# Optimization experiments

Measured on AMD Instinct MI355X. Metric: run time of the kernel, lower is better.

The kernel has to match this reference:

```python
import jax, jax.numpy as jnp
import numpy as np

DIL = 2  # dilation_rate from init_kwargs

def _conv_same(x, w, b, dil=DIL):
    # x: [B,H,W,C], w: [kh,kw,Cin,Cout] (HWIO), 'same' padding with dilation, stride 1
    y = jax.lax.conv_general_dilated(
        x, w, window_strides=(1, 1), padding='SAME',
        rhs_dilation=(dil, dil),
        dimension_numbers=('NHWC', 'HWIO', 'NHWC'))
    return y + b


def setup_inputs() -> dict:
    key = jax.random.key(0)
    ks = jax.random.split(key, 4)
    B, H, W, C = 8, 128, 256, 64
    F, VF, K = 64, 64, 3
    X = jax.random.normal(ks[0], (B, H, W, C), dtype=jnp.float32)
    Wq = jax.random.normal(ks[1], (K, K, C, F), dtype=jnp.float32) * 0.05
    Wk = jax.random.normal(ks[2], (K, K, C, F), dtype=jnp.float32) * 0.05
    Wv = jax.random.normal(ks[3], (K, K, C, VF), dtype=jnp.float32) * 0.05
    bq = jnp.zeros((F,), jnp.float32)
    bk = jnp.zeros((F,), jnp.float32)
    bv = jnp.zeros((VF,), jnp.float32)
    return {"X": X, "Wq": Wq, "bq": bq, "Wk": Wk, "bk": bk, "Wv": Wv, "bv": bv}


def reference(X, Wq, bq, Wk, bk, Wv, bv):
    q = _conv_same(X, Wq, bq)   # [B,H,W,F]
    k = _conv_same(X, Wk, bk)   # [B,H,W,F]
    v = _conv_same(X, Wv, bv)   # [B,H,W,VF]
    # tf.matmul(q, k, transpose_b=True): batch dims [B,H], attend along W. No scaling.
    scores = jnp.einsum('bhqf,bhkf->bhqk', q, k)          # [B,H,W,W]
    attn = jax.nn.softmax(scores, axis=-1)
    return jnp.einsum('bhqk,bhkf->bhqf', attn, v)         # [B,H,W,VF]
```

## Files before the change

### kernel.cpp

```cpp
#include <hip/hip_runtime.h>

#define B_ 8
#define H_ 128
#define W_ 256
#define C_ 64
#define F_ 64

typedef __attribute__((ext_vector_type(8))) short short8;
typedef __attribute__((ext_vector_type(8))) _Float16 half8;
typedef __attribute__((ext_vector_type(4))) float f32x4;

__device__ __forceinline__ unsigned short f2h(float x) {
    _Float16 h = (_Float16)x;
    return __builtin_bit_cast(unsigned short, h);
}

__device__ __forceinline__ f32x4 mfma16(short8 a, short8 b, f32x4 c) {
    return __builtin_amdgcn_mfma_f32_16x16x32_f16(
        __builtin_bit_cast(half8, a), __builtin_bit_cast(half8, b), c, 0, 0, 0);
}

__global__ void wprep_kernel(const float* __restrict__ Wq,
                             const float* __restrict__ Wk,
                             const float* __restrict__ Wv,
                             unsigned short* __restrict__ Wt)
{
    int e = blockIdx.x * 256 + threadIdx.x;
    int c   = e & 63;
    int f   = (e >> 6) % 192;
    int tap = e / 12288;
    const float* src = (f < 64) ? Wq : (f < 128) ? Wk : Wv;
    int ff = f & 63;
    float v = src[(long)tap * 4096 + c * 64 + ff];
    Wt[e] = f2h(v);
}

#define XST 36
#define WST 36

__global__ __launch_bounds__(256, 3) void conv_mfma(
    const float* __restrict__ X, const unsigned short* __restrict__ Wt,
    const float* __restrict__ bq, const float* __restrict__ bk,
    const float* __restrict__ bv,
    unsigned short* __restrict__ Qg, unsigned short* __restrict__ Kg,
    unsigned short* __restrict__ Vtg)
{
    __shared__ __align__(16) unsigned short Xs[260 * XST];
    __shared__ __align__(16) unsigned short Wls[288 * WST];

    const int tid  = threadIdx.x;
    const int wv   = tid >> 6;
    const int lane = tid & 63;
    const int l15  = lane & 15;
    const int g    = lane >> 4;
    const int bx   = blockIdx.x;
    const int bh   = bx >> 1;
    const int half = bx & 1;
    const int b    = bh >> 7;
    const int h    = bh & 127;

    f32x4 acc[4][6];
    #pragma unroll
    for (int mt = 0; mt < 4; ++mt)
        #pragma unroll
        for (int nt = 0; nt < 6; ++nt)
            acc[mt][nt] = (f32x4){0.f, 0.f, 0.f, 0.f};

    for (int kh = 0; kh < 3; ++kh) {
        const int ih = h + 2 * (kh - 1);
        if ((unsigned)ih >= (unsigned)H_) continue;
        const float* Xr = X + ((long)(b * H_ + ih) * W_) * C_;

        for (int cc = 0; cc < 2; ++cc) {
            const int c0 = cc * 32;
            __syncthreads();

            for (int e = tid; e < 260 * 8; e += 256) {
                const int row = e >> 3, c4 = e & 7;
                const int w_in = row - 2;
                float4 val = make_float4(0.f, 0.f, 0.f, 0.f);
                if ((unsigned)w_in < (unsigned)W_)
                    val = *(const float4*)(Xr + (long)w_in * 64 + c0 + c4 * 4);
                uint2 p;
                p.x = (unsigned)f2h(val.x) | ((unsigned)f2h(val.y) << 16);
                p.y = (unsigned)f2h(val.z) | ((unsigned)f2h(val.w) << 16);
                *(uint2*)(Xs + row * XST + c4 * 4) = p;
            }
            for (int e = tid; e < 1152; e += 256) {
                const int c8 = e & 3, f = (e >> 2) % 96, kw = e / 384;
                uint4 d = *(const uint4*)(Wt +
                    (((long)(kh * 3 + kw) * 192 + half * 96 + f) * 64 + c0 + c8 * 8));
                *(uint4*)(Wls + (kw * 96 + f) * WST + c8 * 8) = d;
            }
            __syncthreads();

            #pragma unroll
            for (int kw = 0; kw < 3; ++kw) {
                short8 bfrag[6];
                #pragma unroll
                for (int nt = 0; nt < 6; ++nt)
                    bfrag[nt] = *(const short8*)(Wls +
                        (kw * 96 + nt * 16 + l15) * WST + g * 8);
                #pragma unroll
                for (int mt = 0; mt < 4; ++mt) {
                    const int row = wv * 64 + mt * 16 + l15 + 2 * kw;
                    short8 a = *(const short8*)(Xs + row * XST + g * 8);
                    #pragma unroll
                    for (int nt = 0; nt < 6; ++nt)
                        acc[mt][nt] = mfma16(a, bfrag[nt], acc[mt][nt]);
                }
            }
        }
    }

    float bias[6];
    #pragma unroll
    for (int nt = 0; nt < 6; ++nt) {
        const int fp = half * 96 + nt * 16 + l15;
        bias[nt] = (fp < 64) ? bq[fp] : (fp < 128) ? bk[fp - 64] : bv[fp - 128];
    }
    #pragma unroll
    for (int mt = 0; mt < 4; ++mt) {
        const int wrow = wv * 64 + mt * 16 + 4 * g;
        #pragma unroll
        for (int nt = 0; nt < 6; ++nt) {
            const int fp = half * 96 + nt * 16 + l15;
            if (fp < 128) {
                unsigned short* dst = (fp < 64) ? Qg : Kg;
                const int f = fp & 63;
                #pragma unroll
                for (int r = 0; r < 4; ++r)
                    dst[((long)bh * 256 + wrow + r) * 64 + f] =
                        f2h(acc[mt][nt][r] + bias[nt]);
            } else {
                const int f = fp - 128;
                uint2 p;
                p.x = (unsigned)f2h(acc[mt][nt][0] + bias[nt]) |
                      ((unsigned)f2h(acc[mt][nt][1] + bias[nt]) << 16);
                p.y = (unsigned)f2h(acc[mt][nt][2] + bias[nt]) |
                      ((unsigned)f2h(acc[mt][nt][3] + bias[nt]) << 16);
                *(uint2*)(Vtg + ((long)bh * 64 + f) * 256 + wrow) = p;
            }
        }
    }
}

#define KST 72
#define PST 72

__global__ __launch_bounds__(256, 2) void attn_mfma(
    const unsigned short* __restrict__ Qg, const unsigned short* __restrict__ Kg,
    const unsigned short* __restrict__ Vtg, float* __restrict__ Out)
{
    __shared__ __align__(16) unsigned short Ks[2][64 * KST];
    __shared__ __align__(16) unsigned short Vts[2][64 * KST];
    __shared__ __align__(16) unsigned short Ps[4][64 * PST];

    const int tid  = threadIdx.x;
    const int wv   = tid >> 6;
    const int lane = tid & 63;
    const int l15  = lane & 15;
    const int g    = lane >> 4;
    const long bh  = blockIdx.x;

    short8 qf[4][2];
    #pragma unroll
    for (int mt = 0; mt < 4; ++mt)
        #pragma unroll
        for (int kt = 0; kt < 2; ++kt)
            qf[mt][kt] = *(const short8*)(Qg +
                (bh * 256 + wv * 64 + mt * 16 + l15) * 64 + (kt * 4 + g) * 8);

    const int srow = tid >> 2, sch = (tid & 3) * 16;

    {
        const unsigned short* kp = Kg + (bh * 256 + srow) * 64 + sch;
        const unsigned short* vp = Vtg + (bh * 64 + srow) * 256 + sch;
        *(uint4*)(Ks[0] + srow * KST + sch)     = *(const uint4*)(kp);
        *(uint4*)(Ks[0] + srow * KST + sch + 8) = *(const uint4*)(kp + 8);
        *(uint4*)(Vts[0] + srow * KST + sch)     = *(const uint4*)(vp);
        *(uint4*)(Vts[0] + srow * KST + sch + 8) = *(const uint4*)(vp + 8);
    }

    f32x4 po[4][4], lacc[4];
    float mrun[4][4];
    #pragma unroll
    for (int mt = 0; mt < 4; ++mt) {
        #pragma unroll
        for (int nt = 0; nt < 4; ++nt) po[mt][nt] = (f32x4){0.f,0.f,0.f,0.f};
        lacc[mt] = (f32x4){0.f,0.f,0.f,0.f};
        #pragma unroll
        for (int r = 0; r < 4; ++r) mrun[mt][r] = -3.0e38f;
    }

    short8 ones;
    #pragma unroll
    for (int i = 0; i < 8; ++i) ones[i] = (short)0x3C00;

    unsigned short* Pw = &Ps[wv][0];

    for (int t = 0; t < 4; ++t) {
        __syncthreads();
        const int cur = t & 1;
        if (t < 3) {
            const int nx = cur ^ 1, t0 = (t + 1) * 64;
            const unsigned short* kp = Kg + (bh * 256 + t0 + srow) * 64 + sch;
            const unsigned short* vp = Vtg + (bh * 64 + srow) * 256 + t0 + sch;
            *(uint4*)(Ks[nx] + srow * KST + sch)     = *(const uint4*)(kp);
            *(uint4*)(Ks[nx] + srow * KST + sch + 8) = *(const uint4*)(kp + 8);
            *(uint4*)(Vts[nx] + srow * KST + sch)     = *(const uint4*)(vp);
            *(uint4*)(Vts[nx] + srow * KST + sch + 8) = *(const uint4*)(vp + 8);
        }

        f32x4 s[4][4];
        #pragma unroll
        for (int mt = 0; mt < 4; ++mt)
            #pragma unroll
            for (int nt = 0; nt < 4; ++nt) s[mt][nt] = (f32x4){0.f,0.f,0.f,0.f};
        #pragma unroll
        for (int kt = 0; kt < 2; ++kt)
            #pragma unroll
            for (int nt = 0; nt < 4; ++nt) {
                short8 kb = *(const short8*)(Ks[cur] +
                    (nt * 16 + l15) * KST + (kt * 4 + g) * 8);
                #pragma unroll
                for (int mt = 0; mt < 4; ++mt)
                    s[mt][nt] = mfma16(qf[mt][kt], kb, s[mt][nt]);
            }

        #pragma unroll
        for (int mt = 0; mt < 4; ++mt) {
            float tm[4];
            #pragma unroll
            for (int r = 0; r < 4; ++r) {
                float a0 = fmaxf(s[mt][0][r], s[mt][1][r]);
                float a1 = fmaxf(s[mt][2][r], s[mt][3][r]);
                float t0 = fmaxf(a0, a1);
                t0 = fmaxf(t0, __shfl_xor(t0, 1));
                t0 = fmaxf(t0, __shfl_xor(t0, 2));
                t0 = fmaxf(t0, __shfl_xor(t0, 4));
                t0 = fmaxf(t0, __shfl_xor(t0, 8));
                tm[r] = t0;
            }
            float worst = tm[0] - mrun[mt][0];
            #pragma unroll
            for (int r = 1; r < 4; ++r) worst = fmaxf(worst, tm[r] - mrun[mt][r]);
            if (__all(worst <= 8.f)) {
                #pragma unroll
                for (int r = 0; r < 4; ++r) {
                    const float mo = mrun[mt][r];
                    const int wrow = mt * 16 + 4 * g + r;
                    #pragma unroll
                    for (int nt = 0; nt < 4; ++nt)
                        Pw[wrow * PST + nt * 16 + l15] = f2h(__expf(s[mt][nt][r] - mo));
                }
            } else {
                #pragma unroll
                for (int r = 0; r < 4; ++r) {
                    const float mo = mrun[mt][r];
                    const float mn = fmaxf(mo, tm[r]);
                    const float al = __expf(mo - mn);
                    mrun[mt][r] = mn;
                    lacc[mt][r] *= al;
                    #pragma unroll
                    for (int nf = 0; nf < 4; ++nf) po[mt][nf][r] *= al;
                    const int wrow = mt * 16 + 4 * g + r;
                    #pragma unroll
                    for (int nt = 0; nt < 4; ++nt)
                        Pw[wrow * PST + nt * 16 + l15] = f2h(__expf(s[mt][nt][r] - mn));
                }
            }
        }

        #pragma unroll
        for (int kt = 0; kt < 2; ++kt) {
            short8 vb[4];
            #pragma unroll
            for (int nf = 0; nf < 4; ++nf)
                vb[nf] = *(const short8*)(Vts[cur] +
                    (nf * 16 + l15) * KST + (kt * 4 + g) * 8);
            #pragma unroll
            for (int mt = 0; mt < 4; ++mt) {
                short8 pa = *(const short8*)(Pw +
                    (mt * 16 + l15) * PST + (kt * 4 + g) * 8);
                #pragma unroll
                for (int nf = 0; nf < 4; ++nf)
                    po[mt][nf] = mfma16(pa, vb[nf], po[mt][nf]);
                lacc[mt] = mfma16(pa, ones, lacc[mt]);
            }
        }
    }

    #pragma unroll
    for (int mt = 0; mt < 4; ++mt) {
        #pragma unroll
        for (int r = 0; r < 4; ++r) {
            const float inv = 1.0f / lacc[mt][r];
            const long wrow = bh * 256 + wv * 64 + mt * 16 + 4 * g + r;
            #pragma unroll
            for (int nf = 0; nf < 4; ++nf)
                Out[wrow * 64 + nf * 16 + l15] = po[mt][nf][r] * inv;
        }
    }
}

extern "C" void kernel_launch(void* const* d_in, const int* in_sizes, int n_in,
                              void* d_out, int out_size, void* d_ws, size_t ws_size,
                              hipStream_t stream) {
    const float* X  = (const float*)d_in[0];
    const float* Wq = (const float*)d_in[1];
    const float* bq = (const float*)d_in[2];
    const float* Wk = (const float*)d_in[3];
    const float* bk = (const float*)d_in[4];
    const float* Wv = (const float*)d_in[5];
    const float* bv = (const float*)d_in[6];
    float* out = (float*)d_out;

    const size_t NE = (size_t)B_ * H_ * W_ * F_;
    unsigned short* q  = (unsigned short*)d_ws;
    unsigned short* k  = q + NE;
    unsigned short* vt = k + NE;
    unsigned short* wt = vt + NE;

    wprep_kernel<<<432, 256, 0, stream>>>(Wq, Wk, Wv, wt);
    conv_mfma<<<B_ * H_ * 2, 256, 0, stream>>>(X, wt, bq, bk, bv, q, k, vt);
    attn_mfma<<<B_ * H_, 256, 0, stream>>>(q, k, vt, out);
}
```

Before: 336.2 us.

## Split conv and attention blocks along W and prefetch tiles through registers

The conv kernel now splits each row into two W halves, giving four blocks per (b,h). It stages X and weight tiles through registers so the global loads for the next phase overlap the MFMA work on the current one. The attention kernel likewise splits queries into two halves per row, doubling the grid, and replaces its double-buffered LDS with a single buffer filled by register prefetch. Q is pre-scaled by log2(e) so softmax can use exp2f, and the rescale-skip threshold is adjusted to match. The cost is reloading the 2-column X halo and the K/V tiles twice per row, plus an extra barrier per iteration.

```diff
diff --git a/kernel.cpp b/kernel.cpp
--- a/kernel.cpp
+++ b/kernel.cpp
@@ -5,6 +5,7 @@
 #define W_ 256
 #define C_ 64
 #define F_ 64
+#define LOG2E 1.44269504f
 
 typedef __attribute__((ext_vector_type(8))) short short8;
 typedef __attribute__((ext_vector_type(8))) _Float16 half8;
@@ -45,7 +46,7 @@
     unsigned short* __restrict__ Qg, unsigned short* __restrict__ Kg,
     unsigned short* __restrict__ Vtg)
 {
-    __shared__ __align__(16) unsigned short Xs[260 * XST];
+    __shared__ __align__(16) unsigned short Xs[132 * XST];
     __shared__ __align__(16) unsigned short Wls[288 * WST];
 
     const int tid  = threadIdx.x;
@@ -54,63 +55,123 @@
     const int l15  = lane & 15;
     const int g    = lane >> 4;
     const int bx   = blockIdx.x;
-    const int bh   = bx >> 1;
-    const int half = bx & 1;
+    const int bh   = bx >> 2;
+    const int half = (bx >> 1) & 1;
+    const int qh   = bx & 1;
     const int b    = bh >> 7;
     const int h    = bh & 127;
 
-    f32x4 acc[4][6];
-    #pragma unroll
-    for (int mt = 0; mt < 4; ++mt)
+    int khl[3]; int nkh = 0;
+    #pragma unroll
+    for (int kh = 0; kh < 3; ++kh) {
+        const int ih = h + 2 * (kh - 1);
+        if ((unsigned)ih < (unsigned)H_) khl[nkh++] = kh;
+    }
+    const int nph = nkh * 2;
+
+    float4 xv[5];
+    uint4  wv4[5];
+
+    #define CONV_LOAD(p)                                                        \
+    {                                                                           \
+        const int kh_ = khl[(p) >> 1], c0_ = ((p) & 1) * 32;                    \
+        const int ih_ = h + 2 * (kh_ - 1);                                      \
+        const float* Xr_ = X + ((long)(b * H_ + ih_) * W_) * C_;                \
+        _Pragma("unroll")                                                       \
+        for (int it = 0; it < 4; ++it) {                                        \
+            const int e = tid + it * 256;                                       \
+            const int row = e >> 3, c4 = e & 7;                                 \
+            const int w_in = qh * 128 - 2 + row;                                \
+            xv[it] = ((unsigned)w_in < (unsigned)W_)                            \
+                ? *(const float4*)(Xr_ + (long)w_in * 64 + c0_ + c4 * 4)        \
+                : make_float4(0.f, 0.f, 0.f, 0.f);                              \
+        }                                                                       \
+        if (tid < 32) {                                                         \
+            const int e = 1024 + tid;                                           \
+            const int row = e >> 3, c4 = e & 7;                                 \
+            const int w_in = qh * 128 - 2 + row;                                \
+            xv[4] = ((unsigned)w_in < (unsigned)W_)                             \
+                ? *(const float4*)(Xr_ + (long)w_in * 64 + c0_ + c4 * 4)        \
+                : make_float4(0.f, 0.f, 0.f, 0.f);                              \
+        }                                                                       \
+        _Pragma("unroll")                                                       \
+        for (int it = 0; it < 4; ++it) {                                        \
+            const int e = tid + it * 256;                                       \
+            const int c8 = e & 3, f = (e >> 2) % 96, kw = e / 384;              \
+            wv4[it] = *(const uint4*)(Wt +                                      \
+                (((long)(kh_ * 3 + kw) * 192 + half * 96 + f) * 64 + c0_ + c8 * 8)); \
+        }                                                                       \
+        if (tid < 128) {                                                        \
+            const int e = 1024 + tid;                                           \
+            const int c8 = e & 3, f = (e >> 2) % 96, kw = e / 384;              \
+            wv4[4] = *(const uint4*)(Wt +                                       \
+                (((long)(kh_ * 3 + kw) * 192 + half * 96 + f) * 64 + c0_ + c8 * 8)); \
+        }                                                                       \
+    }
+
+    #define CONV_WRITE()                                                        \
+    {                                                                           \
+        _Pragma("unroll")                                                       \
+        for (int it = 0; it < 4; ++it) {                                        \
+            const int e = tid + it * 256;                                       \
+            const int row = e >> 3, c4 = e & 7;                                 \
+            uint2 p_;                                                           \
+            p_.x = (unsigned)f2h(xv[it].x) | ((unsigned)f2h(xv[it].y) << 16);   \
+            p_.y = (unsigned)f2h(xv[it].z) | ((unsigned)f2h(xv[it].w) << 16);   \
+            *(uint2*)(Xs + row * XST + c4 * 4) = p_;                            \
+        }                                                                       \
+        if (tid < 32) {                                                         \
+            const int e = 1024 + tid;                                           \
+            const int row = e >> 3, c4 = e & 7;                                 \
+            uint2 p_;                                                           \
+            p_.x = (unsigned)f2h(xv[4].x) | ((unsigned)f2h(xv[4].y) << 16);     \
+            p_.y = (unsigned)f2h(xv[4].z) | ((unsigned)f2h(xv[4].w) << 16);     \
+            *(uint2*)(Xs + row * XST + c4 * 4) = p_;                            \
+        }                                                                       \
+        _Pragma("unroll")                                                       \
+        for (int it = 0; it < 4; ++it) {                                        \
+            const int e = tid + it * 256;                                       \
+            const int c8 = e & 3, f = (e >> 2) % 96, kw = e / 384;              \
+            *(uint4*)(Wls + (kw * 96 + f) * WST + c8 * 8) = wv4[it];            \
+        }                                                                       \
+        if (tid < 128) {                                                        \
+            const int e = 1024 + tid;                                           \
+            const int c8 = e & 3, f = (e >> 2) % 96, kw = e / 384;              \
+            *(uint4*)(Wls + (kw * 96 + f) * WST + c8 * 8) = wv4[4];             \
+        }                                                                       \
+    }
+
+    f32x4 acc[2][6];
+    #pragma unroll
+    for (int mt = 0; mt < 2; ++mt)
         #pragma unroll
         for (int nt = 0; nt < 6; ++nt)
             acc[mt][nt] = (f32x4){0.f, 0.f, 0.f, 0.f};
 
-    for (int kh = 0; kh < 3; ++kh) {
-        const int ih = h + 2 * (kh - 1);
-        if ((unsigned)ih >= (unsigned)H_) continue;
-        const float* Xr = X + ((long)(b * H_ + ih) * W_) * C_;
-
-        for (int cc = 0; cc < 2; ++cc) {
-            const int c0 = cc * 32;
-            __syncthreads();
-
-            for (int e = tid; e < 260 * 8; e += 256) {
-                const int row = e >> 3, c4 = e & 7;
-                const int w_in = row - 2;
-                float4 val = make_float4(0.f, 0.f, 0.f, 0.f);
-                if ((unsigned)w_in < (unsigned)W_)
-                    val = *(const float4*)(Xr + (long)w_in * 64 + c0 + c4 * 4);
-                uint2 p;
-                p.x = (unsigned)f2h(val.x) | ((unsigned)f2h(val.y) << 16);
-                p.y = (unsigned)f2h(val.z) | ((unsigned)f2h(val.w) << 16);
-                *(uint2*)(Xs + row * XST + c4 * 4) = p;
-            }
-            for (int e = tid; e < 1152; e += 256) {
-                const int c8 = e & 3, f = (e >> 2) % 96, kw = e / 384;
-                uint4 d = *(const uint4*)(Wt +
-                    (((long)(kh * 3 + kw) * 192 + half * 96 + f) * 64 + c0 + c8 * 8));
-                *(uint4*)(Wls + (kw * 96 + f) * WST + c8 * 8) = d;
-            }
-            __syncthreads();
-
-            #pragma unroll
-            for (int kw = 0; kw < 3; ++kw) {
-                short8 bfrag[6];
+    CONV_LOAD(0);
+
+    for (int p = 0; p < nph; ++p) {
+        CONV_WRITE();
+        __syncthreads();
+        if (p + 1 < nph) CONV_LOAD(p + 1);
+
+        #pragma unroll
+        for (int kw = 0; kw < 3; ++kw) {
+            short8 bfrag[6];
+            #pragma unroll
+            for (int nt = 0; nt < 6; ++nt)
+                bfrag[nt] = *(const short8*)(Wls +
+                    (kw * 96 + nt * 16 + l15) * WST + g * 8);
+            #pragma unroll
+            for (int mt = 0; mt < 2; ++mt) {
+                const int row = wv * 32 + mt * 16 + l15 + 2 * kw;
+                short8 a = *(const short8*)(Xs + row * XST + g * 8);
                 #pragma unroll
                 for (int nt = 0; nt < 6; ++nt)
-                    bfrag[nt] = *(const short8*)(Wls +
-                        (kw * 96 + nt * 16 + l15) * WST + g * 8);
-                #pragma unroll
-                for (int mt = 0; mt < 4; ++mt) {
-                    const int row = wv * 64 + mt * 16 + l15 + 2 * kw;
-                    short8 a = *(const short8*)(Xs + row * XST + g * 8);
-                    #pragma unroll
-                    for (int nt = 0; nt < 6; ++nt)
-                        acc[mt][nt] = mfma16(a, bfrag[nt], acc[mt][nt]);
-                }
+                    acc[mt][nt] = mfma16(a, bfrag[nt], acc[mt][nt]);
             }
         }
+        __syncthreads();
     }
 
     float bias[6];
@@ -120,17 +181,21 @@
         bias[nt] = (fp < 64) ? bq[fp] : (fp < 128) ? bk[fp - 64] : bv[fp - 128];
     }
     #pragma unroll
-    for (int mt = 0; mt < 4; ++mt) {
-        const int wrow = wv * 64 + mt * 16 + 4 * g;
+    for (int mt = 0; mt < 2; ++mt) {
+        const int wrow = qh * 128 + wv * 32 + mt * 16 + 4 * g;
         #pragma unroll
         for (int nt = 0; nt < 6; ++nt) {
             const int fp = half * 96 + nt * 16 + l15;
-            if (fp < 128) {
-                unsigned short* dst = (fp < 64) ? Qg : Kg;
-                const int f = fp & 63;
+            if (fp < 64) {
                 #pragma unroll
                 for (int r = 0; r < 4; ++r)
-                    dst[((long)bh * 256 + wrow + r) * 64 + f] =
+                    Qg[((long)bh * 256 + wrow + r) * 64 + fp] =
+                        f2h((acc[mt][nt][r] + bias[nt]) * LOG2E);
+            } else if (fp < 128) {
+                const int f = fp - 64;
+                #pragma unroll
+                for (int r = 0; r < 4; ++r)
+                    Kg[((long)bh * 256 + wrow + r) * 64 + f] =
                         f2h(acc[mt][nt][r] + bias[nt]);
             } else {
                 const int f = fp - 128;
@@ -152,40 +217,54 @@
     const unsigned short* __restrict__ Qg, const unsigned short* __restrict__ Kg,
     const unsigned short* __restrict__ Vtg, float* __restrict__ Out)
 {
-    __shared__ __align__(16) unsigned short Ks[2][64 * KST];
-    __shared__ __align__(16) unsigned short Vts[2][64 * KST];
-    __shared__ __align__(16) unsigned short Ps[4][64 * PST];
+    __shared__ __align__(16) unsigned short Ks[64 * KST];
+    __shared__ __align__(16) unsigned short Vts[64 * KST];
+    __shared__ __align__(16) unsigned short Ps[4][32 * PST];
 
     const int tid  = threadIdx.x;
     const int wv   = tid >> 6;
     const int lane = tid & 63;
     const int l15  = lane & 15;
     const int g    = lane >> 4;
-    const long bh  = blockIdx.x;
-
-    short8 qf[4][2];
-    #pragma unroll
-    for (int mt = 0; mt < 4; ++mt)
+    const int bx   = blockIdx.x;
+    const long bh  = bx >> 1;
+    const int qh   = bx & 1;
+
+    short8 qf[2][2];
+    #pragma unroll
+    for (int mt = 0; mt < 2; ++mt)
         #pragma unroll
         for (int kt = 0; kt < 2; ++kt)
             qf[mt][kt] = *(const short8*)(Qg +
-                (bh * 256 + wv * 64 + mt * 16 + l15) * 64 + (kt * 4 + g) * 8);
+                (bh * 256 + qh * 128 + wv * 32 + mt * 16 + l15) * 64 + (kt * 4 + g) * 8);
 
     const int srow = tid >> 2, sch = (tid & 3) * 16;
-
-    {
-        const unsigned short* kp = Kg + (bh * 256 + srow) * 64 + sch;
-        const unsigned short* vp = Vtg + (bh * 64 + srow) * 256 + sch;
-        *(uint4*)(Ks[0] + srow * KST + sch)     = *(const uint4*)(kp);
-        *(uint4*)(Ks[0] + srow * KST + sch + 8) = *(const uint4*)(kp + 8);
-        *(uint4*)(Vts[0] + srow * KST + sch)     = *(const uint4*)(vp);
-        *(uint4*)(Vts[0] + srow * KST + sch + 8) = *(const uint4*)(vp + 8);
-    }
-
-    f32x4 po[4][4], lacc[4];
-    float mrun[4][4];
-    #pragma unroll
-    for (int mt = 0; mt < 4; ++mt) {
+    uint4 kreg[2], vreg[2];
+
+    #define ATTN_LOAD(t)                                                        \
+    {                                                                           \
+        const unsigned short* kp = Kg + (bh * 256 + (t) * 64 + srow) * 64 + sch;\
+        const unsigned short* vp = Vtg + (bh * 64 + srow) * 256 + (t) * 64 + sch;\
+        kreg[0] = *(const uint4*)(kp);                                          \
+        kreg[1] = *(const uint4*)(kp + 8);                                      \
+        vreg[0] = *(const uint4*)(vp);                                          \
+        vreg[1] = *(const uint4*)(vp + 8);                                      \
+    }
+    #define ATTN_WRITE()                                                        \
+    {                                                                           \
+        *(uint4*)(Ks + srow * KST + sch)      = kreg[0];                        \
+        *(uint4*)(Ks + srow * KST + sch + 8)  = kreg[1];                        \
+        *(uint4*)(Vts + srow * KST + sch)     = vreg[0];                        \
+        *(uint4*)(Vts + srow * KST + sch + 8) = vreg[1];                        \
+    }
+
+    ATTN_LOAD(0);
+    ATTN_WRITE();
+
+    f32x4 po[2][4], lacc[2];
+    float mrun[2][4];
+    #pragma unroll
+    for (int mt = 0; mt < 2; ++mt) {
         #pragma unroll
         for (int nt = 0; nt < 4; ++nt) po[mt][nt] = (f32x4){0.f,0.f,0.f,0.f};
         lacc[mt] = (f32x4){0.f,0.f,0.f,0.f};
@@ -201,35 +280,26 @@
 
     for (int t = 0; t < 4; ++t) {
         __syncthreads();
-        const int cur = t & 1;
-        if (t < 3) {
-            const int nx = cur ^ 1, t0 = (t + 1) * 64;
-            const unsigned short* kp = Kg + (bh * 256 + t0 + srow) * 64 + sch;
-            const unsigned short* vp = Vtg + (bh * 64 + srow) * 256 + t0 + sch;
-            *(uint4*)(Ks[nx] + srow * KST + sch)     = *(const uint4*)(kp);
-            *(uint4*)(Ks[nx] + srow * KST + sch + 8) = *(const uint4*)(kp + 8);
-            *(uint4*)(Vts[nx] + srow * KST + sch)     = *(const uint4*)(vp);
-            *(uint4*)(Vts[nx] + srow * KST + sch + 8) = *(const uint4*)(vp + 8);
-        }
-
-        f32x4 s[4][4];
-        #pragma unroll
-        for (int mt = 0; mt < 4; ++mt)
+        if (t < 3) ATTN_LOAD(t + 1);
+
+        f32x4 s[2][4];
+        #pragma unroll
+        for (int mt = 0; mt < 2; ++mt)
             #pragma unroll
             for (int nt = 0; nt < 4; ++nt) s[mt][nt] = (f32x4){0.f,0.f,0.f,0.f};
         #pragma unroll
         for (int kt = 0; kt < 2; ++kt)
             #pragma unroll
             for (int nt = 0; nt < 4; ++nt) {
-                short8 kb = *(const short8*)(Ks[cur] +
+                short8 kb = *(const short8*)(Ks +
                     (nt * 16 + l15) * KST + (kt * 4 + g) * 8);
                 #pragma unroll
-                for (int mt = 0; mt < 4; ++mt)
+                for (int mt = 0; mt < 2; ++mt)
                     s[mt][nt] = mfma16(qf[mt][kt], kb, s[mt][nt]);
             }
 
         #pragma unroll
-        for (int mt = 0; mt < 4; ++mt) {
+        for (int mt = 0; mt < 2; ++mt) {
             float tm[4];
             #pragma unroll
             for (int r = 0; r < 4; ++r) {
@@ -245,21 +315,21 @@
             float worst = tm[0] - mrun[mt][0];
             #pragma unroll
             for (int r = 1; r < 4; ++r) worst = fmaxf(worst, tm[r] - mrun[mt][r]);
-            if (__all(worst <= 8.f)) {
+            if (__all(worst <= 11.5f)) {
                 #pragma unroll
                 for (int r = 0; r < 4; ++r) {
                     const float mo = mrun[mt][r];
                     const int wrow = mt * 16 + 4 * g + r;
                     #pragma unroll
                     for (int nt = 0; nt < 4; ++nt)
-                        Pw[wrow * PST + nt * 16 + l15] = f2h(__expf(s[mt][nt][r] - mo));
+                        Pw[wrow * PST + nt * 16 + l15] = f2h(exp2f(s[mt][nt][r] - mo));
                 }
             } else {
                 #pragma unroll
                 for (int r = 0; r < 4; ++r) {
                     const float mo = mrun[mt][r];
                     const float mn = fmaxf(mo, tm[r]);
-                    const float al = __expf(mo - mn);
+                    const float al = exp2f(mo - mn);
                     mrun[mt][r] = mn;
                     lacc[mt][r] *= al;
                     #pragma unroll
@@ -267,7 +337,7 @@
                     const int wrow = mt * 16 + 4 * g + r;
                     #pragma unroll
                     for (int nt = 0; nt < 4; ++nt)
-                        Pw[wrow * PST + nt * 16 + l15] = f2h(__expf(s[mt][nt][r] - mn));
+                        Pw[wrow * PST + nt * 16 + l15] = f2h(exp2f(s[mt][nt][r] - mn));
                 }
             }
         }
@@ -277,10 +347,10 @@
             short8 vb[4];
             #pragma unroll
             for (int nf = 0; nf < 4; ++nf)
-                vb[nf] = *(const short8*)(Vts[cur] +
+                vb[nf] = *(const short8*)(Vts +
                     (nf * 16 + l15) * KST + (kt * 4 + g) * 8);
             #pragma unroll
-            for (int mt = 0; mt < 4; ++mt) {
+            for (int mt = 0; mt < 2; ++mt) {
                 short8 pa = *(const short8*)(Pw +
                     (mt * 16 + l15) * PST + (kt * 4 + g) * 8);
                 #pragma unroll
@@ -289,14 +359,17 @@
                 lacc[mt] = mfma16(pa, ones, lacc[mt]);
             }
         }
-    }
-
-    #pragma unroll
-    for (int mt = 0; mt < 4; ++mt) {
+
+        __syncthreads();
+        if (t < 3) ATTN_WRITE();
+    }
+
+    #pragma unroll
+    for (int mt = 0; mt < 2; ++mt) {
         #pragma unroll
         for (int r = 0; r < 4; ++r) {
             const float inv = 1.0f / lacc[mt][r];
-            const long wrow = bh * 256 + wv * 64 + mt * 16 + 4 * g + r;
+            const long wrow = bh * 256 + qh * 128 + wv * 32 + mt * 16 + 4 * g + r;
             #pragma unroll
             for (int nf = 0; nf < 4; ++nf)
                 Out[wrow * 64 + nf * 16 + l15] = po[mt][nf][r] * inv;
@@ -323,6 +396,6 @@
     unsigned short* wt = vt + NE;
 
     wprep_kernel<<<432, 256, 0, stream>>>(Wq, Wk, Wv, wt);
-    conv_mfma<<<B_ * H_ * 2, 256, 0, stream>>>(X, wt, bq, bk, bv, q, k, vt);
-    attn_mfma<<<B_ * H_, 256, 0, stream>>>(q, k, vt, out);
-}
+    conv_mfma<<<B_ * H_ * 4, 256, 0, stream>>>(X, wt, bq, bk, bv, q, k, vt);
+    attn_mfma<<<B_ * H_ * 2, 256, 0, stream>>>(q, k, vt, out);
+}
```

Result: slower. 383.1 us (+13.9%).
